# Performance work log

Measured on AMD Instinct MI355X. Metric: run time of the kernel, lower is better.

## Reference

```python
import jax, jax.numpy as jnp
import numpy as np

N_NODES = 100000
N_EDGES = 1600000
D_IN, D_HID, D_OUT = 32, 16, 2


def graph_conv(x, edge_index, w_rel, w_root, b):
    # PyG GraphConv (aggr='add'): out_i = x_i @ W_root^T + (sum_{j in N(i)} x_j) @ W_rel^T + b
    src, dst = edge_index[0], edge_index[1]
    msgs = x[src]                                            # [E, d] neighbor gather
    agg = jax.ops.segment_sum(msgs, dst, num_segments=N_NODES)  # [N, d] scatter-add
    return agg @ w_rel.T + x @ w_root.T + b


def setup_inputs() -> dict:
    key = jax.random.key(0)
    ks = jax.random.split(key, 8)
    x = jax.random.normal(ks[0], (N_NODES, D_IN), dtype=jnp.float32)
    edge_index = jax.random.randint(ks[1], (2, N_EDGES), 0, N_NODES, dtype=jnp.int64)
    def glorot(k, shape):
        lim = np.sqrt(6.0 / (shape[0] + shape[1]))
        return jax.random.uniform(k, shape, jnp.float32, -lim, lim)
    w1_rel = glorot(ks[2], (D_HID, D_IN))
    w1_root = glorot(ks[3], (D_HID, D_IN))
    b1 = jnp.zeros((D_HID,), jnp.float32)
    w2_rel = glorot(ks[4], (D_OUT, D_HID))
    w2_root = glorot(ks[5], (D_OUT, D_HID))
    b2 = jnp.zeros((D_OUT,), jnp.float32)
    return {"x": x, "edge_index": edge_index,
            "w1_rel": w1_rel, "w1_root": w1_root, "b1": b1,
            "w2_rel": w2_rel, "w2_root": w2_root, "b2": b2}


def reference(x, edge_index, w1_rel, w1_root, b1, w2_rel, w2_root, b2):
    h = graph_conv(x, edge_index, w1_rel, w1_root, b1)
    h = jax.nn.relu(h)
    out = graph_conv(h, edge_index, w2_rel, w2_root, b2)
    return out
```

## Files before the change

### kernel.cpp

```cpp
#include <hip/hip_runtime.h>

#define N_NODES 100000
#define N_EDGES 1600000
#define D_IN 32
#define D_HID 16
#define D_OUT 2

#define NPB 128
#define NB 782
#define NROWS (NB * NPB)
#define CHUNK 6400
#define BBLOCKS 250
#define EPT 13

#define PBC 2560
#define DUMMY_SRC 100000u
#define DUMMY_REC ((127u << 17) | DUMMY_SRC)


__device__ __forceinline__ unsigned bfr(float x) {
    unsigned u = __float_as_uint(x);
    return (u + 0x7FFFu + ((u >> 16) & 1u)) >> 16;
}
__device__ __forceinline__ float bfu(unsigned lo16) {
    return __uint_as_float(lo16 << 16);
}

__global__ __launch_bounds__(512) void k_bin_node1(
    const int* __restrict__ ei, const float* __restrict__ x,
    const float* __restrict__ w_rel, const float* __restrict__ w_root,
    const float* __restrict__ bb,
    unsigned short* __restrict__ xr, float* __restrict__ agg,
    int* __restrict__ gcur, unsigned* __restrict__ recs2)
{
    __shared__ int cnt[NB];
    __shared__ int loff[NB];
    __shared__ int gbase[NB];
    __shared__ unsigned sorted[CHUNK];
    __shared__ unsigned short bkt16[CHUNK];
    __shared__ float s_rel[D_HID * D_IN];
    __shared__ float s_root[D_HID * D_IN];
    __shared__ float s_b[D_HID];
    int blk = blockIdx.x, tid = threadIdx.x;
    int e0 = blk * CHUNK;

    int srcs[EPT], dsts[EPT];
#pragma unroll
    for (int k = 0; k < EPT; k++) {
        int off = tid + k * 512;
        bool ok = off < CHUNK;
        int e = e0 + off;
        srcs[k] = ok ? ei[e] : 0;
        dsts[k] = ok ? ei[N_EDGES + e] : -1;
    }

    for (int i = tid; i < D_HID * D_IN; i += 512) {
        s_rel[i]  = w_rel[i];
        s_root[i] = w_root[i];
    }
    if (tid < D_HID) s_b[tid] = bb[tid];
    for (int i = tid; i < NB; i += 512) cnt[i] = 0;
    __syncthreads();

    int rank[EPT];
#pragma unroll
    for (int k = 0; k < EPT; k++)
        rank[k] = (dsts[k] >= 0) ? atomicAdd(&cnt[dsts[k] >> 7], 1) : 0;

    int node = blk * 512 + tid;
    if (node == N_NODES) {
        uint4* xp = (uint4*)(xr + (size_t)node * D_HID);
        xp[0] = make_uint4(0, 0, 0, 0);
        xp[1] = make_uint4(0, 0, 0, 0);
    } else if (node < N_NODES) {
        float row[D_IN];
        const float4* xp = (const float4*)(x + (size_t)node * D_IN);
#pragma unroll
        for (int i = 0; i < D_IN / 4; i++) {
            float4 v = xp[i];
            row[4*i+0] = v.x; row[4*i+1] = v.y; row[4*i+2] = v.z; row[4*i+3] = v.w;
        }
        float oa[D_HID], orr[D_HID];
#pragma unroll
        for (int o = 0; o < D_HID; o++) {
            float a = 0.f, r = s_b[o];
#pragma unroll
            for (int k = 0; k < D_IN; k++) {
                a += row[k] * s_rel[o * D_IN + k];
                r += row[k] * s_root[o * D_IN + k];
            }
            oa[o] = a; orr[o] = r;
        }
        unsigned p[8];
#pragma unroll
        for (int i = 0; i < 8; i++)
            p[i] = bfr(oa[2*i]) | (bfr(oa[2*i+1]) << 16);
        uint4* xrp = (uint4*)(xr + (size_t)node * D_HID);
        xrp[0] = make_uint4(p[0], p[1], p[2], p[3]);
        xrp[1] = make_uint4(p[4], p[5], p[6], p[7]);
        float4* aggp = (float4*)(agg + (size_t)node * D_HID);
#pragma unroll
        for (int i = 0; i < D_HID / 4; i++)
            aggp[i] = make_float4(orr[4*i], orr[4*i+1], orr[4*i+2], orr[4*i+3]);
    }
    __syncthreads();

    if (tid < 64) {
        int running = 0;
        for (int c = 0; c < (NB + 63) / 64; c++) {
            int idx = c * 64 + tid;
            int v = (idx < NB) ? cnt[idx] : 0;
            int incl = v;
#pragma unroll
            for (int off = 1; off < 64; off <<= 1) {
                int t = __shfl_up(incl, off);
                if (tid >= off) incl += t;
            }
            if (idx < NB) loff[idx] = running + incl - v;
            running += __shfl(incl, 63);
        }
    } else {
        for (int i = tid - 64; i < NB; i += 448)
            gbase[i] = (cnt[i] > 0) ? atomicAdd(&gcur[i], cnt[i]) : 0;
    }
    __syncthreads();

#pragma unroll
    for (int k = 0; k < EPT; k++) {
        if (dsts[k] >= 0) {
            int bkt = dsts[k] >> 7;
            int p = loff[bkt] + rank[k];
            sorted[p] = ((unsigned)(dsts[k] & (NPB - 1)) << 17) | (unsigned)srcs[k];
            bkt16[p] = (unsigned short)bkt;
        }
    }
    __syncthreads();

    for (int i = tid; i < CHUNK; i += 512) {
        int b = bkt16[i];
        int idx = gbase[b] + (i - loff[b]);
        if (idx < PBC)
            recs2[b * PBC + idx] = sorted[i];
    }
}

__global__ __launch_bounds__(512) void k_sortacc(
    const int* __restrict__ gcur, unsigned* __restrict__ recs2,
    const unsigned short* __restrict__ srcf, const float* __restrict__ agg,
    const float* __restrict__ w_rel2, const float* __restrict__ w_root2,
    const float* __restrict__ bb2,
    float* __restrict__ hr, float* __restrict__ outv,
    unsigned* __restrict__ bbase)
{
    __shared__ unsigned stage[PBC];
    __shared__ unsigned sorted[PBC];
    __shared__ int hist[NPB], base[NPB];
    __shared__ float s_rel2[D_OUT * D_HID];
    __shared__ float s_root2[D_OUT * D_HID];
    __shared__ float s_b2[D_OUT];
    int b = blockIdx.x, tid = threadIdx.x;
    int n = min(gcur[b], PBC);
    unsigned* w = recs2 + (size_t)b * PBC;

    if (tid < D_OUT * D_HID) {
        s_rel2[tid]  = w_rel2[tid];
        s_root2[tid] = w_root2[tid];
    }
    if (tid < D_OUT) s_b2[tid] = bb2[tid];

    if (tid < NPB) hist[tid] = 0;
    for (int i = tid; i < n; i += 512) stage[i] = w[i];
    __syncthreads();

    unsigned rc[PBC / 512];
    int rk[PBC / 512];
#pragma unroll
    for (int j = 0; j < PBC / 512; j++) {
        int i = tid + j * 512;
        if (i < n) {
            rc[j] = stage[i];
            rk[j] = atomicAdd(&hist[rc[j] >> 17], 1);
        } else {
            rc[j] = DUMMY_REC; rk[j] = -1;
        }
    }
    __syncthreads();

    if (tid < 64) {
        int v0 = hist[tid], v1 = hist[tid + 64];
        int s0 = v0, s1 = v1;
#pragma unroll
        for (int off = 1; off < 64; off <<= 1) {
            int t0 = __shfl_up(s0, off);
            int t1 = __shfl_up(s1, off);
            if (tid >= off) { s0 += t0; s1 += t1; }
        }
        int tot0 = __shfl(s0, 63);
        base[tid]      = s0 - v0;
        base[tid + 64] = tot0 + s1 - v1;
    }
    __syncthreads();

#pragma unroll
    for (int j = 0; j < PBC / 512; j++) {
        if (rk[j] >= 0)
            sorted[base[rc[j] >> 17] + rk[j]] = rc[j];
    }
    __syncthreads();

    for (int i = tid; i < n; i += 512) w[i] = sorted[i];
    if (tid < NPB)
        bbase[b * NPB + tid] = (unsigned)base[tid] | ((unsigned)hist[tid] << 16);

    int t = tid >> 2, l = tid & 3;
    int node = b * NPB + t;
    int cbase = base[t], c = hist[t];
    float acc0, acc1, acc2_, acc3;
    if (node < N_NODES) {
        const float4 r4 = *(const float4*)(agg + (size_t)node * D_HID + l * 4);
        acc0 = r4.x; acc1 = r4.y; acc2_ = r4.z; acc3 = r4.w;
    } else {
        acc0 = acc1 = acc2_ = acc3 = 0.f;
    }
    for (int r0 = 0; r0 < c; r0 += 8) {
        int m = c - r0;
        uint2 vv[8];
#pragma unroll
        for (int j = 0; j < 8; j++) {
            unsigned src = (j < m) ? (sorted[cbase + r0 + j] & 0x1FFFF) : DUMMY_SRC;
            vv[j] = *(const uint2*)(srcf + (size_t)src * D_HID + l * 4);
        }
#pragma unroll
        for (int j = 0; j < 8; j++) {
            acc0 += bfu(vv[j].x & 0xFFFFu); acc1 += bfu(vv[j].x >> 16);
            acc2_ += bfu(vv[j].y & 0xFFFFu); acc3 += bfu(vv[j].y >> 16);
        }
    }

    float h0 = fmaxf(acc0, 0.f), h1 = fmaxf(acc1, 0.f);
    float h2 = fmaxf(acc2_, 0.f), h3 = fmaxf(acc3, 0.f);
    float pr[D_OUT], pp[D_OUT];
#pragma unroll
    for (int o = 0; o < D_OUT; o++) {
        const float* wr = &s_rel2[o * D_HID + l * 4];
        const float* wo = &s_root2[o * D_HID + l * 4];
        pr[o] = h0 * wr[0] + h1 * wr[1] + h2 * wr[2] + h3 * wr[3];
        pp[o] = h0 * wo[0] + h1 * wo[1] + h2 * wo[2] + h3 * wo[3];
    }
#pragma unroll
    for (int m = 1; m < 4; m <<= 1) {
        pr[0] += __shfl_xor(pr[0], m); pr[1] += __shfl_xor(pr[1], m);
        pp[0] += __shfl_xor(pp[0], m); pp[1] += __shfl_xor(pp[1], m);
    }
    if (l == 0) {
        if (node < N_NODES) {
            ((float2*)hr)[node]   = make_float2(pr[0], pr[1]);
            ((float2*)outv)[node] = make_float2(pp[0] + s_b2[0], pp[1] + s_b2[1]);
        } else if (node == N_NODES) {
            ((float2*)hr)[node] = make_float2(0.f, 0.f);
        }
    }
}

__global__ __launch_bounds__(256) void k_acc2(
    const unsigned* __restrict__ recs2, const unsigned* __restrict__ bbase,
    const float* __restrict__ hr, float* __restrict__ outv)
{
    __shared__ unsigned srt[PBC];
    int b = blockIdx.x, tid = threadIdx.x;
    unsigned pk127 = bbase[b * NPB + 127];
    int n = (int)(pk127 & 0xFFFFu) + (int)(pk127 >> 16);
    const unsigned* rp = recs2 + (size_t)b * PBC;
    for (int i = tid; i < n; i += 256) srt[i] = rp[i];

    int t = tid >> 1, l = tid & 1;
    unsigned pk = bbase[b * NPB + t];
    int cbase = (int)(pk & 0xFFFFu), c = (int)(pk >> 16);
    int node = b * NPB + t;
    __syncthreads();

    float acc = 0.f;
    for (int r0 = 0; r0 < c; r0 += 8) {
        int m = c - r0;
        float vv[8];
#pragma unroll
        for (int j = 0; j < 8; j++) {
            unsigned src = (j < m) ? (srt[cbase + r0 + j] & 0x1FFFF) : DUMMY_SRC;
            vv[j] = hr[(size_t)src * D_OUT + l];
        }
#pragma unroll
        for (int j = 0; j < 8; j++) acc += vv[j];
    }
    if (node < N_NODES)
        outv[(size_t)node * D_OUT + l] += acc;
}

extern "C" void kernel_launch(void* const* d_in, const int* in_sizes, int n_in,
                              void* d_out, int out_size, void* d_ws, size_t ws_size,
                              hipStream_t stream) {
    const float* x       = (const float*)d_in[0];
    const int*   ei      = (const int*)  d_in[1];
    const float* w1_rel  = (const float*)d_in[2];
    const float* w1_root = (const float*)d_in[3];
    const float* b1      = (const float*)d_in[4];
    const float* w2_rel  = (const float*)d_in[5];
    const float* w2_root = (const float*)d_in[6];
    const float* b2      = (const float*)d_in[7];
    float* out = (float*)d_out;

    float*          agg   = (float*)d_ws;
    unsigned short* xrh   = (unsigned short*)(agg + (size_t)NROWS * D_HID);
    unsigned*       recs2 = (unsigned*)(xrh + (size_t)NROWS * D_HID);
    float*          hr    = (float*)(recs2 + (size_t)NB * PBC);
    unsigned*       bbase = (unsigned*)(hr + (size_t)NROWS * D_OUT);
    int*            gcur  = (int*)(bbase + (size_t)NROWS);

    hipMemsetAsync(gcur, 0, NB * sizeof(int), stream);

    k_bin_node1<<<dim3(BBLOCKS), dim3(512), 0, stream>>>(
        ei, x, w1_rel, w1_root, b1, xrh, agg, gcur, recs2);

    k_sortacc<<<dim3(NB), dim3(512), 0, stream>>>(
        gcur, recs2, xrh, agg, w2_rel, w2_root, b2, hr, out, bbase);

    k_acc2<<<dim3(NB), dim3(256), 0, stream>>>(recs2, bbase, hr, out);
}
```

Baseline: 134.9 us.

## Replace LDS atomic histograms with wave-ballot ranking and restructure second-layer gather

Replaces the shared-memory atomicAdd bucket counting in both sorting kernels with a per-wave match-by-ballot ranking (waveRank), keeping one histogram column per wave. Prefix scans now run over the bucket×wave table to get per-wave offsets. This removes contended LDS atomics but adds one ballot per key bit, and the binning kernel's per-wave table needs more shared memory. The final layer kernel also drops its LDS staging, using four lanes per node that read record indices straight from global memory, load float2 rows, and combine partial sums with shuffles.

```diff
diff --git a/kernel.cpp b/kernel.cpp
--- a/kernel.cpp
+++ b/kernel.cpp
@@ -24,6 +24,25 @@
 }
 __device__ __forceinline__ float bfu(unsigned lo16) {
     return __uint_as_float(lo16 << 16);
+}
+
+template <int NBITS, int STRIDE>
+__device__ __forceinline__ int waveRank(int key, bool valid, int* whCol, int lane) {
+    unsigned long long m = __ballot(valid);
+#pragma unroll
+    for (int b = 0; b < NBITS; b++) {
+        unsigned long long bal = __ballot((key >> b) & 1);
+        m &= ((key >> b) & 1) ? bal : ~bal;
+    }
+    int rk = -1;
+    if (valid) {
+        unsigned long long below = (1ull << lane) - 1ull;
+        int before = whCol[key * STRIDE];
+        rk = before + __popcll(m & below);
+        if ((m & below) == 0ull)
+            whCol[key * STRIDE] = before + __popcll(m);
+    }
+    return rk;
 }
 
 __global__ __launch_bounds__(512) void k_bin_node1(
@@ -33,8 +52,8 @@
     unsigned short* __restrict__ xr, float* __restrict__ agg,
     int* __restrict__ gcur, unsigned* __restrict__ recs2)
 {
+    __shared__ int wh2[NB * 9];
     __shared__ int cnt[NB];
-    __shared__ int loff[NB];
     __shared__ int gbase[NB];
     __shared__ unsigned sorted[CHUNK];
     __shared__ unsigned short bkt16[CHUNK];
@@ -42,6 +61,7 @@
     __shared__ float s_root[D_HID * D_IN];
     __shared__ float s_b[D_HID];
     int blk = blockIdx.x, tid = threadIdx.x;
+    int w = tid >> 6, lane = tid & 63;
     int e0 = blk * CHUNK;
 
     int srcs[EPT], dsts[EPT];
@@ -59,13 +79,16 @@
         s_root[i] = w_root[i];
     }
     if (tid < D_HID) s_b[tid] = bb[tid];
-    for (int i = tid; i < NB; i += 512) cnt[i] = 0;
+    for (int i = tid; i < NB * 9; i += 512) wh2[i] = 0;
     __syncthreads();
 
     int rank[EPT];
 #pragma unroll
-    for (int k = 0; k < EPT; k++)
-        rank[k] = (dsts[k] >= 0) ? atomicAdd(&cnt[dsts[k] >> 7], 1) : 0;
+    for (int k = 0; k < EPT; k++) {
+        bool valid = dsts[k] >= 0;
+        int key = valid ? (dsts[k] >> 7) : 0;
+        rank[k] = waveRank<10, 9>(key, valid, wh2 + w, lane);
+    }
 
     int node = blk * 512 + tid;
     if (node == N_NODES) {
@@ -105,19 +128,28 @@
     }
     __syncthreads();
 
+    for (int i = tid; i < NB; i += 512) {
+        int t = 0;
+#pragma unroll
+        for (int j = 0; j < 8; j++) t += wh2[i * 9 + j];
+        cnt[i] = t;
+    }
+    __syncthreads();
+
     if (tid < 64) {
         int running = 0;
-        for (int c = 0; c < (NB + 63) / 64; c++) {
-            int idx = c * 64 + tid;
-            int v = (idx < NB) ? cnt[idx] : 0;
-            int incl = v;
+        for (int c0 = 0; c0 < NB * 8; c0 += 64) {
+            int f = c0 + lane;
+            int addr = 0, v = 0;
+            if (f < NB * 8) { addr = (f >> 3) * 9 + (f & 7); v = wh2[addr]; }
+            int s = v;
 #pragma unroll
             for (int off = 1; off < 64; off <<= 1) {
-                int t = __shfl_up(incl, off);
-                if (tid >= off) incl += t;
+                int t = __shfl_up(s, off);
+                if (lane >= off) s += t;
             }
-            if (idx < NB) loff[idx] = running + incl - v;
-            running += __shfl(incl, 63);
+            if (f < NB * 8) wh2[addr] = running + s - v;
+            running += __shfl(s, 63);
         }
     } else {
         for (int i = tid - 64; i < NB; i += 448)
@@ -129,7 +161,7 @@
     for (int k = 0; k < EPT; k++) {
         if (dsts[k] >= 0) {
             int bkt = dsts[k] >> 7;
-            int p = loff[bkt] + rank[k];
+            int p = wh2[bkt * 9 + w] + rank[k];
             sorted[p] = ((unsigned)(dsts[k] & (NPB - 1)) << 17) | (unsigned)srcs[k];
             bkt16[p] = (unsigned short)bkt;
         }
@@ -138,7 +170,7 @@
 
     for (int i = tid; i < CHUNK; i += 512) {
         int b = bkt16[i];
-        int idx = gbase[b] + (i - loff[b]);
+        int idx = gbase[b] + (i - wh2[b * 9]);
         if (idx < PBC)
             recs2[b * PBC + idx] = sorted[i];
     }
@@ -154,22 +186,22 @@
 {
     __shared__ unsigned stage[PBC];
     __shared__ unsigned sorted[PBC];
-    __shared__ int hist[NPB], base[NPB];
+    __shared__ int wh[NPB * 9];
     __shared__ float s_rel2[D_OUT * D_HID];
     __shared__ float s_root2[D_OUT * D_HID];
     __shared__ float s_b2[D_OUT];
     int b = blockIdx.x, tid = threadIdx.x;
+    int w = tid >> 6, lane = tid & 63;
     int n = min(gcur[b], PBC);
-    unsigned* w = recs2 + (size_t)b * PBC;
+    unsigned* wg = recs2 + (size_t)b * PBC;
 
     if (tid < D_OUT * D_HID) {
         s_rel2[tid]  = w_rel2[tid];
         s_root2[tid] = w_root2[tid];
     }
     if (tid < D_OUT) s_b2[tid] = bb2[tid];
-
-    if (tid < NPB) hist[tid] = 0;
-    for (int i = tid; i < n; i += 512) stage[i] = w[i];
+    for (int i = tid; i < NPB * 9; i += 512) wh[i] = 0;
+    for (int i = tid; i < n; i += 512) stage[i] = wg[i];
     __syncthreads();
 
     unsigned rc[PBC / 512];
@@ -177,44 +209,49 @@
 #pragma unroll
     for (int j = 0; j < PBC / 512; j++) {
         int i = tid + j * 512;
-        if (i < n) {
-            rc[j] = stage[i];
-            rk[j] = atomicAdd(&hist[rc[j] >> 17], 1);
-        } else {
-            rc[j] = DUMMY_REC; rk[j] = -1;
-        }
+        bool valid = i < n;
+        rc[j] = valid ? stage[i] : DUMMY_REC;
+        int key = valid ? (int)(rc[j] >> 17) : 0;
+        rk[j] = waveRank<7, 9>(key, valid, wh + w, lane);
     }
     __syncthreads();
 
     if (tid < 64) {
-        int v0 = hist[tid], v1 = hist[tid + 64];
-        int s0 = v0, s1 = v1;
-#pragma unroll
-        for (int off = 1; off < 64; off <<= 1) {
-            int t0 = __shfl_up(s0, off);
-            int t1 = __shfl_up(s1, off);
-            if (tid >= off) { s0 += t0; s1 += t1; }
-        }
-        int tot0 = __shfl(s0, 63);
-        base[tid]      = s0 - v0;
-        base[tid + 64] = tot0 + s1 - v1;
+        int running = 0;
+        for (int c0 = 0; c0 < NPB * 8; c0 += 64) {
+            int f = c0 + lane;
+            int addr = (f >> 3) * 9 + (f & 7);
+            int v = wh[addr];
+            int s = v;
+#pragma unroll
+            for (int off = 1; off < 64; off <<= 1) {
+                int t = __shfl_up(s, off);
+                if (lane >= off) s += t;
+            }
+            wh[addr] = running + s - v;
+            running += __shfl(s, 63);
+        }
     }
     __syncthreads();
 
 #pragma unroll
     for (int j = 0; j < PBC / 512; j++) {
         if (rk[j] >= 0)
-            sorted[base[rc[j] >> 17] + rk[j]] = rc[j];
-    }
-    __syncthreads();
-
-    for (int i = tid; i < n; i += 512) w[i] = sorted[i];
-    if (tid < NPB)
-        bbase[b * NPB + tid] = (unsigned)base[tid] | ((unsigned)hist[tid] << 16);
+            sorted[wh[(rc[j] >> 17) * 9 + w] + rk[j]] = rc[j];
+    }
+    __syncthreads();
+
+    for (int i = tid; i < n; i += 512) wg[i] = sorted[i];
+    if (tid < NPB) {
+        int b0 = wh[tid * 9];
+        int b1 = (tid < NPB - 1) ? wh[(tid + 1) * 9] : n;
+        bbase[b * NPB + tid] = (unsigned)b0 | ((unsigned)(b1 - b0) << 16);
+    }
 
     int t = tid >> 2, l = tid & 3;
     int node = b * NPB + t;
-    int cbase = base[t], c = hist[t];
+    int cbase = wh[t * 9];
+    int c = ((t < NPB - 1) ? wh[(t + 1) * 9] : n) - cbase;
     float acc0, acc1, acc2_, acc3;
     if (node < N_NODES) {
         const float4 r4 = *(const float4*)(agg + (size_t)node * D_HID + l * 4);
@@ -262,37 +299,39 @@
     }
 }
 
-__global__ __launch_bounds__(256) void k_acc2(
+__global__ __launch_bounds__(512) void k_acc2(
     const unsigned* __restrict__ recs2, const unsigned* __restrict__ bbase,
     const float* __restrict__ hr, float* __restrict__ outv)
 {
-    __shared__ unsigned srt[PBC];
     int b = blockIdx.x, tid = threadIdx.x;
-    unsigned pk127 = bbase[b * NPB + 127];
-    int n = (int)(pk127 & 0xFFFFu) + (int)(pk127 >> 16);
-    const unsigned* rp = recs2 + (size_t)b * PBC;
-    for (int i = tid; i < n; i += 256) srt[i] = rp[i];
-
-    int t = tid >> 1, l = tid & 1;
+    int t = tid >> 2, l = tid & 3;
     unsigned pk = bbase[b * NPB + t];
     int cbase = (int)(pk & 0xFFFFu), c = (int)(pk >> 16);
     int node = b * NPB + t;
-    __syncthreads();
-
-    float acc = 0.f;
-    for (int r0 = 0; r0 < c; r0 += 8) {
-        int m = c - r0;
-        float vv[8];
-#pragma unroll
-        for (int j = 0; j < 8; j++) {
-            unsigned src = (j < m) ? (srt[cbase + r0 + j] & 0x1FFFF) : DUMMY_SRC;
-            vv[j] = hr[(size_t)src * D_OUT + l];
-        }
-#pragma unroll
-        for (int j = 0; j < 8; j++) acc += vv[j];
-    }
-    if (node < N_NODES)
-        outv[(size_t)node * D_OUT + l] += acc;
+    const unsigned* rp = recs2 + (size_t)b * PBC;
+
+    float ax = 0.f, ay = 0.f;
+    for (int r0 = 0; r0 < c; r0 += 16) {
+        unsigned s4[4];
+#pragma unroll
+        for (int j = 0; j < 4; j++) {
+            int idx = r0 + j * 4 + l;
+            s4[j] = (idx < c) ? (rp[cbase + idx] & 0x1FFFF) : DUMMY_SRC;
+        }
+        float2 v4[4];
+#pragma unroll
+        for (int j = 0; j < 4; j++) v4[j] = ((const float2*)hr)[s4[j]];
+#pragma unroll
+        for (int j = 0; j < 4; j++) { ax += v4[j].x; ay += v4[j].y; }
+    }
+#pragma unroll
+    for (int m = 1; m < 4; m <<= 1) {
+        ax += __shfl_xor(ax, m); ay += __shfl_xor(ay, m);
+    }
+    if (l == 0 && node < N_NODES) {
+        float2 o = ((const float2*)outv)[node];
+        ((float2*)outv)[node] = make_float2(o.x + ax, o.y + ay);
+    }
 }
 
 extern "C" void kernel_launch(void* const* d_in, const int* in_sizes, int n_in,
@@ -323,5 +362,5 @@
     k_sortacc<<<dim3(NB), dim3(512), 0, stream>>>(
         gcur, recs2, xrh, agg, w2_rel, w2_root, b2, hr, out, bbase);
 
-    k_acc2<<<dim3(NB), dim3(256), 0, stream>>>(recs2, bbase, hr, out);
-}
+    k_acc2<<<dim3(NB), dim3(512), 0, stream>>>(recs2, bbase, hr, out);
+}
```

New measurement: 161.5 us. +19.7%, slower.
